# Optimization experiments

Hardware: AMD Instinct MI355X
Metric: run time of the kernel (lower is better)

Reference implementation:

```python
import jax, jax.numpy as jnp
import numpy as np

B_IMG, P, C, H, W = 32, 2, 128, 56, 56
b = B_IMG * P * P


def setup_inputs() -> dict:
    key = jax.random.key(0)
    ks = jax.random.split(key, 9)
    inp = {"x": jax.random.normal(ks[0], (b, C, H, W), dtype=jnp.float32)}
    names = ["topW", "botW", "leftW", "rightW", "topleftW", "toprightW", "botleftW", "botrightW"]
    for i, n in enumerate(names):
        inp[n] = jax.random.uniform(ks[i + 1], (C,), dtype=jnp.float32)
    inp["padding"] = 1
    inp["num_patches"] = P
    return inp


def reference(x, topW, botW, leftW, rightW, topleftW, toprightW, botleftW, botrightW, padding, num_patches):
    # padding is fixed to 1 (the 2-wide boundary convs emit exactly 1 row/col).
    bb, Cc, Hh, Ww = x.shape
    Pn = num_patches
    # Depthwise boundary "convs": per-channel weighted sum of the 2 boundary rows/cols.
    top_pad = topW[None, :, None] * (x[:, :, 0, :] + x[:, :, 1, :])          # [b,C,W]
    bot_pad = botW[None, :, None] * (x[:, :, Hh - 2, :] + x[:, :, Hh - 1, :])  # [b,C,W]
    left_pad = leftW[None, :, None] * (x[:, :, :, 0] + x[:, :, :, 1])        # [b,C,H]
    right_pad = rightW[None, :, None] * (x[:, :, :, Ww - 2] + x[:, :, :, Ww - 1])  # [b,C,H]

    y = jnp.pad(x, ((0, 0), (0, 0), (1, 1), (1, 1)))  # [b,C,H+2,W+2]
    y = y.at[:, :, 0, 1:Ww + 1].set(top_pad)
    y = y.at[:, :, Hh + 1, 1:Ww + 1].set(bot_pad)
    y = y.at[:, :, 1:Hh + 1, 0].set(left_pad)
    y = y.at[:, :, 1:Hh + 1, Ww + 1].set(right_pad)
    # Corners: padded[1,1]==x[0,0] etc. are untouched by the edge writes.
    y = y.at[:, :, 0, 0].set(topleftW[None, :] * x[:, :, 0, 0])
    y = y.at[:, :, 0, Ww + 1].set(toprightW[None, :] * x[:, :, 0, Ww - 1])
    y = y.at[:, :, Hh + 1, 0].set(botleftW[None, :] * x[:, :, Hh - 1, 0])
    y = y.at[:, :, Hh + 1, Ww + 1].set(botrightW[None, :] * x[:, :, Hh - 1, Ww - 1])

    # Patch-boundary zeroing masks (patches at the true image border get zero pad).
    idx = jnp.arange(bb)
    within = idx % (Pn * Pn)
    top_m = within < Pn
    bot_m = within >= Pn * Pn - Pn
    left_m = (idx % Pn) == 0
    right_m = (idx % Pn) == Pn - 1
    rows = jnp.arange(Hh + 2)
    cols = jnp.arange(Ww + 2)
    zero = ((top_m[:, None, None] & (rows == 0)[None, :, None])
            | (bot_m[:, None, None] & (rows == Hh + 1)[None, :, None])
            | (left_m[:, None, None] & (cols == 0)[None, None, :])
            | (right_m[:, None, None] & (cols == Ww + 1)[None, None, :]))  # [b,H+2,W+2]
    return jnp.where(zero[:, None, :, :], jnp.zeros((), x.dtype), y)
```

## Files before the change

### kernel.cpp

```cpp
#include <hip/hip_runtime.h>

constexpr int B  = 128;
constexpr int C  = 128;
constexpr int H  = 56, W = 56;
constexpr int HO = H + 2, WO = W + 2;
constexpr int PLANE_IN  = H * W;
constexpr int PLANE_OUT = HO * WO;

__global__ __launch_bounds__(256) void pad2d_kernel(
    const float* __restrict__ x,
    const float* __restrict__ topW, const float* __restrict__ botW,
    const float* __restrict__ leftW, const float* __restrict__ rightW,
    const float* __restrict__ tlW,  const float* __restrict__ trW,
    const float* __restrict__ blW,  const float* __restrict__ brW,
    const int* __restrict__ np_ptr,
    float* __restrict__ out)
{
    const int plane = blockIdx.x;
    const int b   = plane / C;
    const int c   = plane - b * C;
    const int tid = threadIdx.x;

    const int Pn = *np_ptr;
    const int within = b % (Pn * Pn);
    const bool top_z   = within < Pn;
    const bool bot_z   = within >= Pn * Pn - Pn;
    const bool left_z  = (b % Pn) == 0;
    const bool right_z = (b % Pn) == Pn - 1;

    const float* __restrict__ xin = x + (size_t)plane * PLANE_IN;
    float* __restrict__ o = out + (size_t)plane * PLANE_OUT;

    const float4* __restrict__ x4 = (const float4*)xin;
    constexpr int NV = H * (W / 4);
    for (int i = tid; i < NV; i += 256) {
        const int r = i / 14;
        const int q = i - r * 14;
        const float4 v = x4[i];
        float* dst = o + (r + 1) * WO + 1 + q * 4;
        dst[0] = v.x; dst[1] = v.y; dst[2] = v.z; dst[3] = v.w;
    }

    if (tid < 228) {
        if (tid < 56) {
            const int col = tid;
            const float v = top_z ? 0.f
                : topW[c] * (xin[col] + xin[W + col]);
            o[col + 1] = v;
        } else if (tid < 112) {
            const int col = tid - 56;
            const float v = bot_z ? 0.f
                : botW[c] * (xin[(H - 2) * W + col] + xin[(H - 1) * W + col]);
            o[(HO - 1) * WO + col + 1] = v;
        } else if (tid < 168) {
            const int r = tid - 112;
            const float v = left_z ? 0.f
                : leftW[c] * (xin[r * W] + xin[r * W + 1]);
            o[(r + 1) * WO] = v;
        } else if (tid < 224) {
            const int r = tid - 168;
            const float v = right_z ? 0.f
                : rightW[c] * (xin[r * W + W - 2] + xin[r * W + W - 1]);
            o[(r + 1) * WO + WO - 1] = v;
        } else if (tid == 224) {
            o[0] = (top_z || left_z) ? 0.f : tlW[c] * xin[0];
        } else if (tid == 225) {
            o[WO - 1] = (top_z || right_z) ? 0.f : trW[c] * xin[W - 1];
        } else if (tid == 226) {
            o[(HO - 1) * WO] = (bot_z || left_z) ? 0.f : blW[c] * xin[(H - 1) * W];
        } else {
            o[(HO - 1) * WO + WO - 1] =
                (bot_z || right_z) ? 0.f : brW[c] * xin[(H - 1) * W + W - 1];
        }
    }
}

extern "C" void kernel_launch(void* const* d_in, const int* in_sizes, int n_in,
                              void* d_out, int out_size, void* d_ws, size_t ws_size,
                              hipStream_t stream) {
    const float* x      = (const float*)d_in[0];
    const float* topW   = (const float*)d_in[1];
    const float* botW   = (const float*)d_in[2];
    const float* leftW  = (const float*)d_in[3];
    const float* rightW = (const float*)d_in[4];
    const float* tlW    = (const float*)d_in[5];
    const float* trW    = (const float*)d_in[6];
    const float* blW    = (const float*)d_in[7];
    const float* brW    = (const float*)d_in[8];
    const int* np_ptr   = (const int*)d_in[10];
    float* out = (float*)d_out;

    pad2d_kernel<<<dim3(B * C), dim3(256), 0, stream>>>(
        x, topW, botW, leftW, rightW, tlW, trW, blW, brW, np_ptr, out);
}
```

Measured before the change: 401.6 us.

## Write output plane with aligned float4 stores computing borders per element

Each thread now produces one aligned float4 of the output plane and computes every element from a gather function. That function handles interior copies, edge sums and corners in one place, which replaces the scalar interior stores and the separate border-writing pass. The goal is fully coalesced 16-byte writes with no second pass over the border. In exchange, input reads become unaligned scalar gathers and every element pays per-element branching. The per-channel weights are also loaded once up front.

```diff
diff --git a/kernel.cpp b/kernel.cpp
--- a/kernel.cpp
+++ b/kernel.cpp
@@ -6,6 +6,7 @@
 constexpr int HO = H + 2, WO = W + 2;
 constexpr int PLANE_IN  = H * W;
 constexpr int PLANE_OUT = HO * WO;
+constexpr int NV4       = PLANE_OUT / 4;
 
 __global__ __launch_bounds__(256) void pad2d_kernel(
     const float* __restrict__ x,
@@ -23,55 +24,50 @@
 
     const int Pn = *np_ptr;
     const int within = b % (Pn * Pn);
-    const bool top_z   = within < Pn;
-    const bool bot_z   = within >= Pn * Pn - Pn;
-    const bool left_z  = (b % Pn) == 0;
-    const bool right_z = (b % Pn) == Pn - 1;
+    const bool tz = within < Pn;
+    const bool bz = within >= Pn * Pn - Pn;
+    const bool lz = (b % Pn) == 0;
+    const bool rz = (b % Pn) == Pn - 1;
+
+    const float tw = topW[c],  bw = botW[c];
+    const float lw = leftW[c], rw = rightW[c];
+    const float tl = tlW[c],   tr = trW[c];
+    const float bl = blW[c],   br = brW[c];
 
     const float* __restrict__ xin = x + (size_t)plane * PLANE_IN;
-    float* __restrict__ o = out + (size_t)plane * PLANE_OUT;
+    float4* __restrict__ o4 = (float4*)(out + (size_t)plane * PLANE_OUT);
 
-    const float4* __restrict__ x4 = (const float4*)xin;
-    constexpr int NV = H * (W / 4);
-    for (int i = tid; i < NV; i += 256) {
-        const int r = i / 14;
-        const int q = i - r * 14;
-        const float4 v = x4[i];
-        float* dst = o + (r + 1) * WO + 1 + q * 4;
-        dst[0] = v.x; dst[1] = v.y; dst[2] = v.z; dst[3] = v.w;
-    }
+    auto elem = [&](int r, int cc) -> float {
+        if ((r >= 1) & (r <= H) & (cc >= 1) & (cc <= W))
+            return xin[(r - 1) * W + (cc - 1)];
+        if (r == 0) {
+            if (cc == 0)      return (tz | lz) ? 0.f : tl * xin[0];
+            if (cc == WO - 1) return (tz | rz) ? 0.f : tr * xin[W - 1];
+            return tz ? 0.f : tw * (xin[cc - 1] + xin[W + cc - 1]);
+        }
+        if (r == HO - 1) {
+            if (cc == 0)      return (bz | lz) ? 0.f : bl * xin[(H - 1) * W];
+            if (cc == WO - 1) return (bz | rz) ? 0.f : br * xin[(H - 1) * W + W - 1];
+            return bz ? 0.f : bw * (xin[(H - 2) * W + cc - 1] + xin[(H - 1) * W + cc - 1]);
+        }
+        if (cc == 0)
+            return lz ? 0.f : lw * (xin[(r - 1) * W] + xin[(r - 1) * W + 1]);
+        return rz ? 0.f : rw * (xin[(r - 1) * W + W - 2] + xin[(r - 1) * W + W - 1]);
+    };
 
-    if (tid < 228) {
-        if (tid < 56) {
-            const int col = tid;
-            const float v = top_z ? 0.f
-                : topW[c] * (xin[col] + xin[W + col]);
-            o[col + 1] = v;
-        } else if (tid < 112) {
-            const int col = tid - 56;
-            const float v = bot_z ? 0.f
-                : botW[c] * (xin[(H - 2) * W + col] + xin[(H - 1) * W + col]);
-            o[(HO - 1) * WO + col + 1] = v;
-        } else if (tid < 168) {
-            const int r = tid - 112;
-            const float v = left_z ? 0.f
-                : leftW[c] * (xin[r * W] + xin[r * W + 1]);
-            o[(r + 1) * WO] = v;
-        } else if (tid < 224) {
-            const int r = tid - 168;
-            const float v = right_z ? 0.f
-                : rightW[c] * (xin[r * W + W - 2] + xin[r * W + W - 1]);
-            o[(r + 1) * WO + WO - 1] = v;
-        } else if (tid == 224) {
-            o[0] = (top_z || left_z) ? 0.f : tlW[c] * xin[0];
-        } else if (tid == 225) {
-            o[WO - 1] = (top_z || right_z) ? 0.f : trW[c] * xin[W - 1];
-        } else if (tid == 226) {
-            o[(HO - 1) * WO] = (bot_z || left_z) ? 0.f : blW[c] * xin[(H - 1) * W];
-        } else {
-            o[(HO - 1) * WO + WO - 1] =
-                (bot_z || right_z) ? 0.f : brW[c] * xin[(H - 1) * W + W - 1];
-        }
+    for (int v = tid; v < NV4; v += 256) {
+        const int j0 = v * 4;
+        int r  = j0 / WO;
+        int cc = j0 - r * WO;
+        float4 ov;
+        ov.x = elem(r, cc);
+        ++cc; if (cc == WO) { cc = 0; ++r; }
+        ov.y = elem(r, cc);
+        ++cc; if (cc == WO) { cc = 0; ++r; }
+        ov.z = elem(r, cc);
+        ++cc; if (cc == WO) { cc = 0; ++r; }
+        ov.w = elem(r, cc);
+        o4[v] = ov;
     }
 }
 
```

Result: no change. 397.8 us (-0.9%).
